# Optimization experiments

Measured on AMD Instinct MI355X. Metric: run time of the kernel, lower is better.

The kernel has to match this reference:

```python
import jax, jax.numpy as jnp
import numpy as np

HID = 512      # hidden_dim
MID = 256      # hid_dim
COND_D = 256   # condition_op_dim
OP_D = 32      # operator_len
EX_D = 32      # extra_info_num
L, N, T = 16, 1024, 8
EPS = 1e-5


def _lstm_cell(x_proj, h, c, Whh, bhh):
    # x_proj: precomputed x @ Wih.T + bih, shape [B, 4H]
    gates = x_proj + h @ Whh.T + bhh
    i, f, g, o = jnp.split(gates, 4, axis=-1)
    i = jax.nn.sigmoid(i); f = jax.nn.sigmoid(f)
    g = jnp.tanh(g); o = jax.nn.sigmoid(o)
    c = f * c + i * g
    h = o * jnp.tanh(c)
    return h, c


def _batchnorm(x, gamma, beta):
    mu = x.mean(0)
    var = x.var(0)  # biased, matches PyTorch training-mode normalization
    return gamma * (x - mu) * jax.lax.rsqrt(var + EPS) + beta


def setup_inputs() -> dict:
    key = jax.random.key(0)
    ks = jax.random.split(key, 24)
    s = lambda *sh: 0.05
    inp = {
        'operators': jax.random.normal(ks[0], (L, N, OP_D), jnp.float32),
        'extra_infos': jax.random.normal(ks[1], (L, N, EX_D), jnp.float32),
        'conditions': jax.random.normal(ks[2], (L, N, T, COND_D), jnp.float32),
        'condition_masks': jnp.ones((L, N, 1), jnp.float32),
        'mapping': jax.random.randint(ks[3], (L, N, 2), 0, N + 1, jnp.int32).astype(jnp.int64),
        'lstm1_Wih': jax.random.normal(ks[4], (4 * HID, COND_D), jnp.float32) * 0.05,
        'lstm1_Whh': jax.random.normal(ks[5], (4 * HID, HID), jnp.float32) * 0.05,
        'lstm1_bih': jnp.zeros((4 * HID,), jnp.float32),
        'lstm1_bhh': jnp.zeros((4 * HID,), jnp.float32),
        'cond_W': jax.random.normal(ks[6], (MID, HID), jnp.float32) * 0.05,
        'cond_b': jnp.zeros((MID,), jnp.float32),
        'bn1_g': jnp.ones((MID,), jnp.float32),
        'bn1_b': jnp.zeros((MID,), jnp.float32),
        'lstm2_Wih': jax.random.normal(ks[7], (4 * HID, OP_D + EX_D + MID), jnp.float32) * 0.05,
        'lstm2_Whh': jax.random.normal(ks[8], (4 * HID, HID), jnp.float32) * 0.05,
        'lstm2_bih': jnp.zeros((4 * HID,), jnp.float32),
        'lstm2_bhh': jnp.zeros((4 * HID,), jnp.float32),
        'bn2_g': jnp.ones((HID,), jnp.float32),
        'bn2_b': jnp.zeros((HID,), jnp.float32),
    }
    return inp


def reference(operators, extra_infos, conditions, condition_masks, mapping,
              lstm1_Wih, lstm1_Whh, lstm1_bih, lstm1_bhh,
              cond_W, cond_b, bn1_g, bn1_b,
              lstm2_Wih, lstm2_Whh, lstm2_bih, lstm2_bhh,
              bn2_g, bn2_b):
    B = L * N
    x = conditions.reshape(B, T, COND_D)
    # lstm1 over conditions; precompute input projections for all steps
    xp = jnp.einsum('btd,gd->btg', x, lstm1_Wih) + lstm1_bih  # [B,T,4H]

    def step1(carry, xt):
        h, c = carry
        h, c = _lstm_cell(xt, h, c, lstm1_Whh, lstm1_bhh)
        return (h, c), None

    h0 = jnp.zeros((B, HID), xp.dtype)
    (h1, _), _ = jax.lax.scan(step1, (h0, h0), jnp.swapaxes(xp, 0, 1))

    last = jax.nn.relu(h1 @ cond_W.T + cond_b)       # [B, MID]
    last = _batchnorm(last, bn1_g, bn1_b).reshape(L, N, MID)

    out = jnp.concatenate([operators, extra_infos, last], axis=2)  # [L,N,IN2]
    xp2 = jnp.einsum('lnd,gd->lng', out, lstm2_Wih) + lstm2_bih    # [L,N,4H]

    hz = jnp.zeros((N, HID), xp2.dtype)
    h, c = _lstm_cell(xp2[L - 1], hz, hz, lstm2_Whh, lstm2_bhh)

    mapping = mapping.astype(jnp.int32)
    levels = jnp.arange(L - 2, -1, -1)

    def tree_step(carry, idx):
        h, c = carry
        mp = mapping[idx]  # [N,2]
        pad = jnp.zeros((1, HID), h.dtype)
        ph = jnp.concatenate([pad, h], 0)  # [N+1,H]
        pc = jnp.concatenate([pad, c], 0)
        h = (ph[mp[:, 0]] + ph[mp[:, 1]]) * 0.5
        c = (pc[mp[:, 0]] + pc[mp[:, 1]]) * 0.5
        h, c = _lstm_cell(xp2[idx], h, c, lstm2_Whh, lstm2_bhh)
        return (h, c), None

    (h, c), _ = jax.lax.scan(tree_step, (h, c), levels)

    # batch_size == N since all operator rows are nonzero
    return _batchnorm(h, bn2_g, bn2_b)  # [N, HID]
```

## Files before the change

kernel.cpp:

```cpp
#include <hip/hip_runtime.h>
#include <hip/hip_bf16.h>
#include <stdint.h>


typedef __bf16 bf16;
typedef __bf16 bf16x8 __attribute__((ext_vector_type(8)));
typedef float f32x4 __attribute__((ext_vector_type(4)));

#define HIDDEN 512

__device__ __forceinline__ float fast_sig(float x) { return 1.f / (1.f + __expf(-x)); }
__device__ __forceinline__ float fast_tanh(float x) {
  float e = __expf(2.f * x);
  return 1.f - 2.f / (e + 1.f);
}

__device__ __forceinline__ void async16(const bf16* g, bf16* l) {
  __builtin_amdgcn_global_load_lds(
      (const __attribute__((address_space(1))) void*)g,
      (__attribute__((address_space(3))) void*)l, 16, 0, 0);
}

__device__ __forceinline__ void cvt_one(const float* __restrict__ src,
                                        bf16* __restrict__ dst, size_t i) {
  float4 a = *(const float4*)(src + i);
  float4 b = *(const float4*)(src + i + 4);
  bf16x8 r;
  r[0] = (bf16)a.x; r[1] = (bf16)a.y; r[2] = (bf16)a.z; r[3] = (bf16)a.w;
  r[4] = (bf16)b.x; r[5] = (bf16)b.y; r[6] = (bf16)b.z; r[7] = (bf16)b.w;
  *(bf16x8*)(dst + i) = r;
}

__global__ void cvt8(const float* __restrict__ src, bf16* __restrict__ dst) {
  size_t i = ((size_t)blockIdx.x * blockDim.x + threadIdx.x) * 8;
  cvt_one(src, dst, i);
}

__global__ void cvt_multi(const float* s0, bf16* d0,
                          const float* s1, bf16* d1,
                          const float* s2, bf16* d2,
                          const float* s3, bf16* d3,
                          const float* s4, bf16* d4,
                          const float* s5, bf16* d5,
                          const float* s6, bf16* d6) {
  int g = blockIdx.x * blockDim.x + threadIdx.x;
  const float* s; bf16* d; int off;
  if      (g < 65536)  { s = s0; d = d0; off = g; }
  else if (g < 131072) { s = s1; d = d1; off = g - 65536; }
  else if (g < 196608) { s = s2; d = d2; off = g - 131072; }
  else if (g < 327680) { s = s3; d = d3; off = g - 196608; }
  else if (g < 344064) { s = s4; d = d4; off = g - 327680; }
  else if (g < 425984) { s = s5; d = d5; off = g - 344064; }
  else if (g < 557056) { s = s6; d = d6; off = g - 425984; }
  else return;
  cvt_one(s, d, (size_t)off * 8);
}

__global__ void detect(const int* __restrict__ map, int* __restrict__ flags) {
  __shared__ int any;
  if (threadIdx.x == 0) any = 0;
  __syncthreads();
  int loc = 0;
  for (int i = threadIdx.x; i < 16384; i += blockDim.x) loc |= map[2 * i + 1];
  if (loc) atomicOr(&any, 1);
  __syncthreads();
  if (threadIdx.x == 0) flags[0] = (any == 0) ? 1 : 0;
}

template <int MT>
__global__ __launch_bounds__(256, 2) void cell_gemm(
    const bf16* __restrict__ A0, int a0off, int a0s, int a0kt,
    const bf16* __restrict__ A1, int a1s, int a1kt,
    const bf16* __restrict__ B0, int b0s,
    const bf16* __restrict__ B1, int b1s,
    const float* __restrict__ bias0, const float* __restrict__ bias1,
    const void* __restrict__ xp_add, int xp_f32,
    const float* __restrict__ c_prev,
    float* __restrict__ c_out,
    bf16* __restrict__ h_b16,
    float* __restrict__ h_f32)
{
  constexpr int BM = MT * 32;
  __shared__ __align__(16) bf16 sA[BM * 64];
  __shared__ __align__(16) bf16 sB[128 * 64];
  const int tid = threadIdx.x;
  const int lane = tid & 63;
  const int quad = lane >> 4, cl = lane & 15;
  const int wave = tid >> 6;
  const int wr = wave >> 1, wc = wave & 1;
  const int bm0 = blockIdx.x * BM;
  const int j0 = blockIdx.y * 32;

  f32x4 acc[MT][4];
#pragma unroll
  for (int mi = 0; mi < MT; ++mi)
#pragma unroll
    for (int g = 0; g < 4; ++g) acc[mi][g] = f32x4{0.f, 0.f, 0.f, 0.f};

#pragma unroll
  for (int ph = 0; ph < 2; ++ph) {
    const int kts = (ph == 0) ? a0kt : a1kt;
    const bf16* ab = (ph == 0) ? A0 : A1;
    const int as = (ph == 0) ? a0s : a1s;
    const int ao = (ph == 0) ? a0off : 0;
    const bf16* bb = (ph == 0) ? B0 : B1;
    const int bs = (ph == 0) ? b0s : b1s;
    for (int kt = 0; kt < kts; ++kt) {
#pragma unroll
      for (int ia = 0; ia < MT; ++ia) {
        int e = ia * 256 + tid;
        int row = e >> 3, sl = e & 7;
        int src = sl ^ (row & 7);
        async16(ab + (size_t)(bm0 + row) * as + ao + kt * 64 + src * 8, sA + e * 8);
      }
#pragma unroll
      for (int ib = 0; ib < 4; ++ib) {
        int e = ib * 256 + tid;
        int row = e >> 3, sl = e & 7;
        int src = sl ^ (row & 7);
        int wrow = (row >> 5) * HIDDEN + j0 + (row & 31);
        async16(bb + (size_t)wrow * bs + kt * 64 + src * 8, sB + e * 8);
      }
      __syncthreads();
#pragma unroll
      for (int kh = 0; kh < 2; ++kh) {
        bf16x8 af[MT], bfr[4];
#pragma unroll
        for (int mi = 0; mi < MT; ++mi) {
          int row = wr * (MT * 16) + mi * 16 + cl;
          int sl = (kh * 4 + quad) ^ (row & 7);
          af[mi] = *(const bf16x8*)&sA[row * 64 + sl * 8];
        }
#pragma unroll
        for (int g = 0; g < 4; ++g) {
          int row = g * 32 + wc * 16 + cl;
          int sl = (kh * 4 + quad) ^ (row & 7);
          bfr[g] = *(const bf16x8*)&sB[row * 64 + sl * 8];
        }
#pragma unroll
        for (int mi = 0; mi < MT; ++mi)
#pragma unroll
          for (int g = 0; g < 4; ++g)
            acc[mi][g] = __builtin_amdgcn_mfma_f32_16x16x32_bf16(af[mi], bfr[g], acc[mi][g], 0, 0, 0);
      }
      __syncthreads();
    }
  }

  const int j = j0 + wc * 16 + cl;
  float bI = bias0[j], bF = bias0[HIDDEN + j];
  float bG = bias0[2 * HIDDEN + j], bO = bias0[3 * HIDDEN + j];
  if (bias1) {
    bI += bias1[j]; bF += bias1[HIDDEN + j];
    bG += bias1[2 * HIDDEN + j]; bO += bias1[3 * HIDDEN + j];
  }
#pragma unroll
  for (int mi = 0; mi < MT; ++mi) {
    int rb = bm0 + wr * (MT * 16) + mi * 16 + quad * 4;
#pragma unroll
    for (int r = 0; r < 4; ++r) {
      int row = rb + r;
      float gi = acc[mi][0][r] + bI;
      float gf = acc[mi][1][r] + bF;
      float gg = acc[mi][2][r] + bG;
      float go = acc[mi][3][r] + bO;
      if (xp_add) {
        size_t base = (size_t)row * 2048;
        if (xp_f32) {
          const float* xr = (const float*)xp_add + base;
          gi += xr[j]; gf += xr[HIDDEN + j];
          gg += xr[2 * HIDDEN + j]; go += xr[3 * HIDDEN + j];
        } else {
          const bf16* xr = (const bf16*)xp_add + base;
          gi += (float)xr[j]; gf += (float)xr[HIDDEN + j];
          gg += (float)xr[2 * HIDDEN + j]; go += (float)xr[3 * HIDDEN + j];
        }
      }
      float iv = fast_sig(gi), fv = fast_sig(gf);
      float gv = fast_tanh(gg), ov = fast_sig(go);
      float cp = c_prev ? c_prev[(size_t)row * HIDDEN + j] : 0.f;
      float cn = fv * cp + iv * gv;
      float hn = ov * fast_tanh(cn);
      c_out[(size_t)row * HIDDEN + j] = cn;
      h_b16[(size_t)row * HIDDEN + j] = (bf16)hn;
      if (h_f32) h_f32[(size_t)row * HIDDEN + j] = hn;
    }
  }
}

template <int MT>
__global__ __launch_bounds__(256, 2) void plain_gemm(
    const bf16* __restrict__ A0, int a0s, int a0kt,
    const bf16* __restrict__ A1, int a1s, int a1kt,
    const bf16* __restrict__ A2, int a2s, int a2kt,
    const bf16* __restrict__ B, int bs,
    const float* __restrict__ bias, int do_relu,
    bf16* __restrict__ outh, float* __restrict__ outf, int Ntot)
{
  constexpr int BM = MT * 32;
  __shared__ __align__(16) bf16 sA[BM * 32];
  __shared__ __align__(16) bf16 sB[128 * 32];
  const int tid = threadIdx.x;
  const int lane = tid & 63;
  const int quad = lane >> 4, cl = lane & 15;
  const int wave = tid >> 6;
  const int wr = wave >> 1, wc = wave & 1;
  const int bm0 = blockIdx.x * BM;
  const int bn0 = blockIdx.y * 128;

  f32x4 acc[MT][4];
#pragma unroll
  for (int mi = 0; mi < MT; ++mi)
#pragma unroll
    for (int ni = 0; ni < 4; ++ni) acc[mi][ni] = f32x4{0.f, 0.f, 0.f, 0.f};

  const int nkt = a0kt + a1kt + a2kt;
  for (int kt = 0; kt < nkt; ++kt) {
    const bf16* abase; int astr, acol;
    if (kt < a0kt)            { abase = A0; astr = a0s; acol = kt * 32; }
    else if (kt < a0kt + a1kt){ abase = A1; astr = a1s; acol = (kt - a0kt) * 32; }
    else                      { abase = A2; astr = a2s; acol = (kt - a0kt - a1kt) * 32; }
#pragma unroll
    for (int ia = 0; ia < MT / 2; ++ia) {
      int e = ia * 256 + tid;
      int row = e >> 2, sl = e & 3;
      int src = sl ^ ((row >> 1) & 3);
      async16(abase + (size_t)(bm0 + row) * astr + acol + src * 8, sA + e * 8);
    }
#pragma unroll
    for (int ib = 0; ib < 2; ++ib) {
      int e = ib * 256 + tid;
      int row = e >> 2, sl = e & 3;
      int src = sl ^ ((row >> 1) & 3);
      async16(B + (size_t)(bn0 + row) * bs + kt * 32 + src * 8, sB + e * 8);
    }
    __syncthreads();
    bf16x8 af[MT], bfr[4];
#pragma unroll
    for (int mi = 0; mi < MT; ++mi) {
      int row = wr * (MT * 16) + mi * 16 + cl;
      int sl = quad ^ ((row >> 1) & 3);
      af[mi] = *(const bf16x8*)&sA[row * 32 + sl * 8];
    }
#pragma unroll
    for (int ni = 0; ni < 4; ++ni) {
      int row = wc * 64 + ni * 16 + cl;
      int sl = quad ^ ((row >> 1) & 3);
      bfr[ni] = *(const bf16x8*)&sB[row * 32 + sl * 8];
    }
#pragma unroll
    for (int mi = 0; mi < MT; ++mi)
#pragma unroll
      for (int ni = 0; ni < 4; ++ni)
        acc[mi][ni] = __builtin_amdgcn_mfma_f32_16x16x32_bf16(af[mi], bfr[ni], acc[mi][ni], 0, 0, 0);
    __syncthreads();
  }

#pragma unroll
  for (int mi = 0; mi < MT; ++mi) {
    int rb = bm0 + wr * (MT * 16) + mi * 16 + quad * 4;
#pragma unroll
    for (int ni = 0; ni < 4; ++ni) {
      int col = bn0 + wc * 64 + ni * 16 + cl;
      float bv = bias ? bias[col] : 0.f;
#pragma unroll
      for (int r = 0; r < 4; ++r) {
        int row = rb + r;
        float v = acc[mi][ni][r] + bv;
        if (do_relu) v = fmaxf(v, 0.f);
        if (outf) outf[(size_t)row * Ntot + col] = v;
        else      outh[(size_t)row * Ntot + col] = (bf16)v;
      }
    }
  }
}

__global__ void gather_h(const int* __restrict__ map, const int* __restrict__ flags,
                         int level,
                         const bf16* __restrict__ h_src, const float* __restrict__ c_src,
                         bf16* __restrict__ hA, float* __restrict__ c_dst)
{
  int n = blockIdx.x, t = threadIdx.x;
  long base = (long)level * 2048 + n * 2;
  int m0, m1;
  if (flags[0]) { m0 = map[base * 2]; m1 = map[base * 2 + 2]; }
  else          { m0 = map[base];     m1 = map[base + 1]; }
  float h0 = m0 ? (float)h_src[(size_t)(m0 - 1) * HIDDEN + t] : 0.f;
  float h1 = m1 ? (float)h_src[(size_t)(m1 - 1) * HIDDEN + t] : 0.f;
  float c0 = m0 ? c_src[(size_t)(m0 - 1) * HIDDEN + t] : 0.f;
  float c1 = m1 ? c_src[(size_t)(m1 - 1) * HIDDEN + t] : 0.f;
  hA[(size_t)n * HIDDEN + t] = (bf16)(0.5f * (h0 + h1));
  c_dst[(size_t)n * HIDDEN + t] = 0.5f * (c0 + c1);
}

__global__ void cell0(const void* __restrict__ xp, int xp_f32,
                      const float* __restrict__ bhh,
                      bf16* __restrict__ h, float* __restrict__ c)
{
  int n = blockIdx.x, j = threadIdx.x;
  float g[4];
#pragma unroll
  for (int k = 0; k < 4; ++k) {
    size_t idx = (size_t)n * 2048 + k * 512 + j;
    float v = xp_f32 ? ((const float*)xp)[idx] : (float)((const bf16*)xp)[idx];
    g[k] = v + bhh[k * 512 + j];
  }
  float cv = fast_sig(g[0]) * fast_tanh(g[2]);
  h[(size_t)n * HIDDEN + j] = (bf16)(fast_sig(g[3]) * fast_tanh(cv));
  c[(size_t)n * HIDDEN + j] = cv;
}

__global__ void bn_reduce_b16(const bf16* __restrict__ x, int rpb, int F,
                              float* __restrict__ partials) {
  int col = threadIdx.x, b = blockIdx.x;
  const bf16* p = x + (size_t)b * rpb * F + col;
  float s = 0.f, q = 0.f;
  for (int r = 0; r < rpb; ++r) { float v = (float)p[(size_t)r * F]; s += v; q += v * v; }
  partials[(size_t)b * 2 * F + col] = s;
  partials[(size_t)b * 2 * F + F + col] = q;
}

__global__ void bn_reduce_f32(const float* __restrict__ x, int rpb, int F,
                              float* __restrict__ partials) {
  int col = threadIdx.x, b = blockIdx.x;
  const float* p = x + (size_t)b * rpb * F + col;
  float s = 0.f, q = 0.f;
  for (int r = 0; r < rpb; ++r) { float v = p[(size_t)r * F]; s += v; q += v * v; }
  partials[(size_t)b * 2 * F + col] = s;
  partials[(size_t)b * 2 * F + F + col] = q;
}

__global__ void bn_final(const float* __restrict__ partials, int nb, int F,
                         const float* __restrict__ g, const float* __restrict__ b,
                         float invB, float* __restrict__ scale, float* __restrict__ shift) {
  int j = threadIdx.x;
  float s = 0.f, q = 0.f;
  for (int i = 0; i < nb; ++i) {
    s += partials[(size_t)i * 2 * F + j];
    q += partials[(size_t)i * 2 * F + F + j];
  }
  float mu = s * invB;
  float var = fmaxf(q * invB - mu * mu, 0.f);
  float sc = g[j] * rsqrtf(var + 1e-5f);
  scale[j] = sc;
  shift[j] = b[j] - sc * mu;
}

__global__ void bn_apply_mid(const bf16* __restrict__ x, const float* __restrict__ scale,
                             const float* __restrict__ shift, int Fmask, size_t total,
                             bf16* __restrict__ out) {
  for (size_t i = blockIdx.x * (size_t)blockDim.x + threadIdx.x; i < total;
       i += (size_t)gridDim.x * blockDim.x) {
    int j = (int)(i & (size_t)Fmask);
    out[i] = (bf16)(scale[j] * (float)x[i] + shift[j]);
  }
}

__global__ void bn_apply_out(const float* __restrict__ x, const float* __restrict__ scale,
                             const float* __restrict__ shift, int Fmask, size_t total,
                             float* __restrict__ out) {
  for (size_t i = blockIdx.x * (size_t)blockDim.x + threadIdx.x; i < total;
       i += (size_t)gridDim.x * blockDim.x) {
    int j = (int)(i & (size_t)Fmask);
    out[i] = scale[j] * x[i] + shift[j];
  }
}

extern "C" void kernel_launch(void* const* d_in, const int* in_sizes, int n_in,
                              void* d_out, int out_size, void* d_ws, size_t ws_size,
                              hipStream_t stream) {
  const float* operators = (const float*)d_in[0];
  const float* extras    = (const float*)d_in[1];
  const float* conds     = (const float*)d_in[2];
  const int*   mapping   = (const int*)d_in[4];
  const float* b1ih = (const float*)d_in[7];
  const float* b1hh = (const float*)d_in[8];
  const float* condb = (const float*)d_in[10];
  const float* bn1g = (const float*)d_in[11];
  const float* bn1b = (const float*)d_in[12];
  const float* b2ih = (const float*)d_in[15];
  const float* b2hh = (const float*)d_in[16];
  const float* bn2g = (const float*)d_in[17];
  const float* bn2b = (const float*)d_in[18];

  char* ws = (char*)d_ws;
  size_t o = 0;
  auto alloc = [&](size_t bytes) {
    char* p = ws + o;
    o += (bytes + 255) & ~(size_t)255;
    return p;
  };
  bf16* conds_b = (bf16*)alloc((size_t)33554432 * 2);
  bf16* ops_b   = (bf16*)alloc((size_t)524288 * 2);
  bf16* ext_b   = (bf16*)alloc((size_t)524288 * 2);
  bf16* w1ih_b  = (bf16*)alloc((size_t)524288 * 2);
  bf16* w1hh_b  = (bf16*)alloc((size_t)1048576 * 2);
  bf16* condw_b = (bf16*)alloc((size_t)131072 * 2);
  bf16* w2ih_b  = (bf16*)alloc((size_t)655360 * 2);
  bf16* w2hh_b  = (bf16*)alloc((size_t)1048576 * 2);
  bf16* h1[2];
  h1[0] = (bf16*)alloc((size_t)16384 * 512 * 2);
  h1[1] = (bf16*)alloc((size_t)16384 * 512 * 2);
  float* c1 = (float*)alloc((size_t)16384 * 512 * 4);
  bf16* last_relu = (bf16*)alloc((size_t)16384 * 256 * 2);
  bf16* last_bn = (bf16*)alloc((size_t)16384 * 256 * 2);
  bf16* h2 = (bf16*)alloc((size_t)1024 * 512 * 2);
  bf16* hA = (bf16*)alloc((size_t)1024 * 512 * 2);
  float* c2a = (float*)alloc((size_t)1024 * 512 * 4);
  float* c2b = (float*)alloc((size_t)1024 * 512 * 4);
  float* h2f = (float*)alloc((size_t)1024 * 512 * 4);
  float* partials = (float*)alloc((size_t)64 * 1024 * 4);
  float* scale1 = (float*)alloc(256 * 4);
  float* shift1 = (float*)alloc(256 * 4);
  float* scale2 = (float*)alloc(512 * 4);
  float* shift2 = (float*)alloc(512 * 4);
  int* flags = (int*)alloc(256);

  size_t xp2_elems = (size_t)16384 * 2048;
  int xpf = (o + xp2_elems * 4 <= ws_size) ? 1 : 0;
  void* xp2 = alloc(xp2_elems * (xpf ? 4 : 2));
  float* xp2f = xpf ? (float*)xp2 : nullptr;
  bf16* xp2h = xpf ? nullptr : (bf16*)xp2;

  detect<<<1, 256, 0, stream>>>(mapping, flags);
  cvt8<<<16384, 256, 0, stream>>>(conds, conds_b);
  cvt_multi<<<2176, 256, 0, stream>>>(
      operators, ops_b, extras, ext_b,
      (const float*)d_in[5], w1ih_b, (const float*)d_in[6], w1hh_b,
      (const float*)d_in[9], condw_b, (const float*)d_in[13], w2ih_b,
      (const float*)d_in[14], w2hh_b);

  for (int t = 0; t < 8; ++t) {
    const bf16* hprev = (t == 0) ? nullptr : h1[t & 1];
    cell_gemm<4><<<dim3(128, 16), 256, 0, stream>>>(
        conds_b, t * 256, 2048, 4,
        hprev, 512, (t == 0) ? 0 : 8,
        w1ih_b, 256, w1hh_b, 512,
        b1ih, b1hh,
        nullptr, 0,
        (t == 0) ? nullptr : c1, c1, h1[(t + 1) & 1], nullptr);
  }

  plain_gemm<2><<<dim3(256, 2), 256, 0, stream>>>(
      h1[0], 512, 16, nullptr, 0, 0, nullptr, 0, 0,
      condw_b, 512, condb, 1, last_relu, nullptr, 256);
  bn_reduce_b16<<<64, 256, 0, stream>>>(last_relu, 256, 256, partials);
  bn_final<<<1, 256, 0, stream>>>(partials, 64, 256, bn1g, bn1b, 1.f / 16384.f, scale1, shift1);
  bn_apply_mid<<<1024, 256, 0, stream>>>(last_relu, scale1, shift1, 255,
                                         (size_t)16384 * 256, last_bn);

  plain_gemm<4><<<dim3(128, 16), 256, 0, stream>>>(
      ops_b, 32, 1, ext_b, 32, 1, last_bn, 256, 8,
      w2ih_b, 320, b2ih, 0, xp2h, xp2f, 2048);

  size_t lvl_sz = (size_t)1024 * 2048;
  const void* xp15 = xpf ? (const void*)(xp2f + 15 * lvl_sz) : (const void*)(xp2h + 15 * lvl_sz);
  cell0<<<1024, 512, 0, stream>>>(xp15, xpf, b2hh, h2, c2a);
  for (int idx = 14; idx >= 0; --idx) {
    gather_h<<<1024, 512, 0, stream>>>(mapping, flags, idx, h2, c2a, hA, c2b);
    const void* xpl = xpf ? (const void*)(xp2f + idx * lvl_sz) : (const void*)(xp2h + idx * lvl_sz);
    cell_gemm<1><<<dim3(32, 16), 256, 0, stream>>>(
        hA, 0, 512, 8,
        nullptr, 0, 0,
        w2hh_b, 512, nullptr, 0,
        b2hh, nullptr,
        xpl, xpf,
        c2b, c2a, h2,
        (idx == 0) ? h2f : nullptr);
  }

  bn_reduce_f32<<<16, 512, 0, stream>>>(h2f, 64, 512, partials);
  bn_final<<<1, 512, 0, stream>>>(partials, 16, 512, bn2g, bn2b, 1.f / 1024.f, scale2, shift2);
  bn_apply_out<<<512, 256, 0, stream>>>(h2f, scale2, shift2, 511,
                                        (size_t)1024 * 512, (float*)d_out);
}
```

Baseline: 1.201 ms.

## Replace per-level tree launches with a persistent kernel using grid barriers

The 15-level tree recurrence becomes one persistent kernel of 512 blocks. Each level gathers parent h into shared memory, runs the recurrent GEMM and fuses the c gather into the cell update, with a global atomic barrier between levels. This replaces about 31 small launches (cell0, gather_h, cell_gemm per level). The three prep kernels are also merged into one launch, and cell_gemm is templated on K-tile counts with its address arithmetic hoisted. The grid barrier assumes all 512 blocks are resident at once, otherwise it deadlocks, and it adds spin-wait cost at each level.

Result: slower. 1.920 ms (+59.8%).

```diff
diff --git a/kernel.cpp b/kernel.cpp
--- a/kernel.cpp
+++ b/kernel.cpp
@@ -8,6 +8,7 @@
 typedef float f32x4 __attribute__((ext_vector_type(4)));
 
 #define HIDDEN 512
+#define TNB 512
 
 __device__ __forceinline__ float fast_sig(float x) { return 1.f / (1.f + __expf(-x)); }
 __device__ __forceinline__ float fast_tanh(float x) {
@@ -31,54 +32,51 @@
   *(bf16x8*)(dst + i) = r;
 }
 
-__global__ void cvt8(const float* __restrict__ src, bf16* __restrict__ dst) {
-  size_t i = ((size_t)blockIdx.x * blockDim.x + threadIdx.x) * 8;
-  cvt_one(src, dst, i);
-}
-
-__global__ void cvt_multi(const float* s0, bf16* d0,
-                          const float* s1, bf16* d1,
-                          const float* s2, bf16* d2,
-                          const float* s3, bf16* d3,
-                          const float* s4, bf16* d4,
-                          const float* s5, bf16* d5,
-                          const float* s6, bf16* d6) {
-  int g = blockIdx.x * blockDim.x + threadIdx.x;
-  const float* s; bf16* d; int off;
-  if      (g < 65536)  { s = s0; d = d0; off = g; }
-  else if (g < 131072) { s = s1; d = d1; off = g - 65536; }
-  else if (g < 196608) { s = s2; d = d2; off = g - 131072; }
-  else if (g < 327680) { s = s3; d = d3; off = g - 196608; }
-  else if (g < 344064) { s = s4; d = d4; off = g - 327680; }
-  else if (g < 425984) { s = s5; d = d5; off = g - 344064; }
-  else if (g < 557056) { s = s6; d = d6; off = g - 425984; }
-  else return;
-  cvt_one(s, d, (size_t)off * 8);
-}
-
-__global__ void detect(const int* __restrict__ map, int* __restrict__ flags) {
-  __shared__ int any;
-  if (threadIdx.x == 0) any = 0;
-  __syncthreads();
-  int loc = 0;
-  for (int i = threadIdx.x; i < 16384; i += blockDim.x) loc |= map[2 * i + 1];
-  if (loc) atomicOr(&any, 1);
-  __syncthreads();
-  if (threadIdx.x == 0) flags[0] = (any == 0) ? 1 : 0;
-}
-
-template <int MT>
+__global__ void prep(const float* conds, bf16* conds_b,
+                     const float* s0, bf16* d0, const float* s1, bf16* d1,
+                     const float* s2, bf16* d2, const float* s3, bf16* d3,
+                     const float* s4, bf16* d4, const float* s5, bf16* d5,
+                     const float* s6, bf16* d6,
+                     const int* map, int* flags, int* bar) {
+  int b = blockIdx.x;
+  int tid = threadIdx.x;
+  if (b < 2176) {
+    int g = b * 256 + tid;
+    const float* s; bf16* d; int off;
+    if      (g < 65536)  { s = s0; d = d0; off = g; }
+    else if (g < 131072) { s = s1; d = d1; off = g - 65536; }
+    else if (g < 196608) { s = s2; d = d2; off = g - 131072; }
+    else if (g < 327680) { s = s3; d = d3; off = g - 196608; }
+    else if (g < 344064) { s = s4; d = d4; off = g - 327680; }
+    else if (g < 425984) { s = s5; d = d5; off = g - 344064; }
+    else if (g < 557056) { s = s6; d = d6; off = g - 425984; }
+    else return;
+    cvt_one(s, d, (size_t)off * 8);
+  } else if (b == 2176) {
+    __shared__ int any;
+    if (tid == 0) { any = 0; bar[0] = 0; bar[1] = 0; }
+    __syncthreads();
+    int loc = 0;
+    for (int i = tid; i < 16384; i += 256) loc |= map[2 * i + 1];
+    if (loc) atomicOr(&any, 1);
+    __syncthreads();
+    if (tid == 0) flags[0] = (any == 0) ? 1 : 0;
+  } else {
+    size_t i = ((size_t)(b - 2177) * 256 + tid) * 8;
+    cvt_one(conds, conds_b, i);
+  }
+}
+
+template <int MT, int KT0, int KT1>
 __global__ __launch_bounds__(256, 2) void cell_gemm(
-    const bf16* __restrict__ A0, int a0off, int a0s, int a0kt,
-    const bf16* __restrict__ A1, int a1s, int a1kt,
+    const bf16* __restrict__ A0, int a0off, int a0s,
+    const bf16* __restrict__ A1, int a1s,
     const bf16* __restrict__ B0, int b0s,
     const bf16* __restrict__ B1, int b1s,
     const float* __restrict__ bias0, const float* __restrict__ bias1,
-    const void* __restrict__ xp_add, int xp_f32,
     const float* __restrict__ c_prev,
     float* __restrict__ c_out,
-    bf16* __restrict__ h_b16,
-    float* __restrict__ h_f32)
+    bf16* __restrict__ h_b16)
 {
   constexpr int BM = MT * 32;
   __shared__ __align__(16) bf16 sA[BM * 64];
@@ -91,99 +89,109 @@
   const int bm0 = blockIdx.x * BM;
   const int j0 = blockIdx.y * 32;
 
+  const bf16* ra[MT][2];
+  const bf16* rb[4][2];
+#pragma unroll
+  for (int mi = 0; mi < MT; ++mi)
+#pragma unroll
+    for (int kh = 0; kh < 2; ++kh) {
+      int row = wr * (MT * 16) + mi * 16 + cl;
+      int sl = (kh * 4 + quad) ^ (row & 7);
+      ra[mi][kh] = &sA[row * 64 + sl * 8];
+    }
+#pragma unroll
+  for (int g = 0; g < 4; ++g)
+#pragma unroll
+    for (int kh = 0; kh < 2; ++kh) {
+      int row = g * 32 + wc * 16 + cl;
+      int sl = (kh * 4 + quad) ^ (row & 7);
+      rb[g][kh] = &sB[row * 64 + sl * 8];
+    }
+
   f32x4 acc[MT][4];
 #pragma unroll
   for (int mi = 0; mi < MT; ++mi)
 #pragma unroll
     for (int g = 0; g < 4; ++g) acc[mi][g] = f32x4{0.f, 0.f, 0.f, 0.f};
 
-#pragma unroll
-  for (int ph = 0; ph < 2; ++ph) {
-    const int kts = (ph == 0) ? a0kt : a1kt;
-    const bf16* ab = (ph == 0) ? A0 : A1;
-    const int as = (ph == 0) ? a0s : a1s;
-    const int ao = (ph == 0) ? a0off : 0;
-    const bf16* bb = (ph == 0) ? B0 : B1;
-    const int bs = (ph == 0) ? b0s : b1s;
-    for (int kt = 0; kt < kts; ++kt) {
-#pragma unroll
-      for (int ia = 0; ia < MT; ++ia) {
-        int e = ia * 256 + tid;
-        int row = e >> 3, sl = e & 7;
-        int src = sl ^ (row & 7);
-        async16(ab + (size_t)(bm0 + row) * as + ao + kt * 64 + src * 8, sA + e * 8);
-      }
-#pragma unroll
-      for (int ib = 0; ib < 4; ++ib) {
-        int e = ib * 256 + tid;
-        int row = e >> 3, sl = e & 7;
-        int src = sl ^ (row & 7);
-        int wrow = (row >> 5) * HIDDEN + j0 + (row & 31);
-        async16(bb + (size_t)wrow * bs + kt * 64 + src * 8, sB + e * 8);
-      }
-      __syncthreads();
-#pragma unroll
-      for (int kh = 0; kh < 2; ++kh) {
-        bf16x8 af[MT], bfr[4];
-#pragma unroll
-        for (int mi = 0; mi < MT; ++mi) {
-          int row = wr * (MT * 16) + mi * 16 + cl;
-          int sl = (kh * 4 + quad) ^ (row & 7);
-          af[mi] = *(const bf16x8*)&sA[row * 64 + sl * 8];
-        }
-#pragma unroll
-        for (int g = 0; g < 4; ++g) {
-          int row = g * 32 + wc * 16 + cl;
-          int sl = (kh * 4 + quad) ^ (row & 7);
-          bfr[g] = *(const bf16x8*)&sB[row * 64 + sl * 8];
-        }
-#pragma unroll
-        for (int mi = 0; mi < MT; ++mi)
-#pragma unroll
-          for (int g = 0; g < 4; ++g)
-            acc[mi][g] = __builtin_amdgcn_mfma_f32_16x16x32_bf16(af[mi], bfr[g], acc[mi][g], 0, 0, 0);
-      }
-      __syncthreads();
-    }
+  const bf16* pa[MT];
+  const bf16* pb[4];
+#pragma unroll
+  for (int ia = 0; ia < MT; ++ia) {
+    int e = ia * 256 + tid, row = e >> 3, sl = e & 7;
+    pa[ia] = A0 + (size_t)((bm0 + row) * a0s + a0off + (sl ^ (row & 7)) * 8);
+  }
+#pragma unroll
+  for (int ib = 0; ib < 4; ++ib) {
+    int e = ib * 256 + tid, row = e >> 3, sl = e & 7;
+    int wrow = (row >> 5) * HIDDEN + j0 + (row & 31);
+    pb[ib] = B0 + (size_t)(wrow * b0s + (sl ^ (row & 7)) * 8);
+  }
+
+  auto ktile = [&]() {
+#pragma unroll
+    for (int ia = 0; ia < MT; ++ia) {
+      async16(pa[ia], sA + (ia * 256 + tid) * 8);
+      pa[ia] += 64;
+    }
+#pragma unroll
+    for (int ib = 0; ib < 4; ++ib) {
+      async16(pb[ib], sB + (ib * 256 + tid) * 8);
+      pb[ib] += 64;
+    }
+    __syncthreads();
+#pragma unroll
+    for (int kh = 0; kh < 2; ++kh) {
+      bf16x8 af[MT], bfr[4];
+#pragma unroll
+      for (int mi = 0; mi < MT; ++mi) af[mi] = *(const bf16x8*)ra[mi][kh];
+#pragma unroll
+      for (int g = 0; g < 4; ++g) bfr[g] = *(const bf16x8*)rb[g][kh];
+#pragma unroll
+      for (int mi = 0; mi < MT; ++mi)
+#pragma unroll
+        for (int g = 0; g < 4; ++g)
+          acc[mi][g] = __builtin_amdgcn_mfma_f32_16x16x32_bf16(af[mi], bfr[g], acc[mi][g], 0, 0, 0);
+    }
+    __syncthreads();
+  };
+
+  for (int kt = 0; kt < KT0; ++kt) ktile();
+  if (KT1 > 0) {
+#pragma unroll
+    for (int ia = 0; ia < MT; ++ia) {
+      int e = ia * 256 + tid, row = e >> 3, sl = e & 7;
+      pa[ia] = A1 + (size_t)((bm0 + row) * a1s + (sl ^ (row & 7)) * 8);
+    }
+#pragma unroll
+    for (int ib = 0; ib < 4; ++ib) {
+      int e = ib * 256 + tid, row = e >> 3, sl = e & 7;
+      int wrow = (row >> 5) * HIDDEN + j0 + (row & 31);
+      pb[ib] = B1 + (size_t)(wrow * b1s + (sl ^ (row & 7)) * 8);
+    }
+    for (int kt = 0; kt < KT1; ++kt) ktile();
   }
 
   const int j = j0 + wc * 16 + cl;
   float bI = bias0[j], bF = bias0[HIDDEN + j];
   float bG = bias0[2 * HIDDEN + j], bO = bias0[3 * HIDDEN + j];
-  if (bias1) {
-    bI += bias1[j]; bF += bias1[HIDDEN + j];
-    bG += bias1[2 * HIDDEN + j]; bO += bias1[3 * HIDDEN + j];
-  }
+  bI += bias1[j]; bF += bias1[HIDDEN + j];
+  bG += bias1[2 * HIDDEN + j]; bO += bias1[3 * HIDDEN + j];
 #pragma unroll
   for (int mi = 0; mi < MT; ++mi) {
-    int rb = bm0 + wr * (MT * 16) + mi * 16 + quad * 4;
+    int rb_ = bm0 + wr * (MT * 16) + mi * 16 + quad * 4;
 #pragma unroll
     for (int r = 0; r < 4; ++r) {
-      int row = rb + r;
-      float gi = acc[mi][0][r] + bI;
-      float gf = acc[mi][1][r] + bF;
-      float gg = acc[mi][2][r] + bG;
-      float go = acc[mi][3][r] + bO;
-      if (xp_add) {
-        size_t base = (size_t)row * 2048;
-        if (xp_f32) {
-          const float* xr = (const float*)xp_add + base;
-          gi += xr[j]; gf += xr[HIDDEN + j];
-          gg += xr[2 * HIDDEN + j]; go += xr[3 * HIDDEN + j];
-        } else {
-          const bf16* xr = (const bf16*)xp_add + base;
-          gi += (float)xr[j]; gf += (float)xr[HIDDEN + j];
-          gg += (float)xr[2 * HIDDEN + j]; go += (float)xr[3 * HIDDEN + j];
-        }
-      }
-      float iv = fast_sig(gi), fv = fast_sig(gf);
-      float gv = fast_tanh(gg), ov = fast_sig(go);
+      int row = rb_ + r;
+      float iv = fast_sig(acc[mi][0][r] + bI);
+      float fv = fast_sig(acc[mi][1][r] + bF);
+      float gv = fast_tanh(acc[mi][2][r] + bG);
+      float ov = fast_sig(acc[mi][3][r] + bO);
       float cp = c_prev ? c_prev[(size_t)row * HIDDEN + j] : 0.f;
       float cn = fv * cp + iv * gv;
       float hn = ov * fast_tanh(cn);
       c_out[(size_t)row * HIDDEN + j] = cn;
       h_b16[(size_t)row * HIDDEN + j] = (bf16)hn;
-      if (h_f32) h_f32[(size_t)row * HIDDEN + j] = hn;
     }
   }
 }
@@ -275,39 +283,151 @@
   }
 }
 
-__global__ void gather_h(const int* __restrict__ map, const int* __restrict__ flags,
-                         int level,
-                         const bf16* __restrict__ h_src, const float* __restrict__ c_src,
-                         bf16* __restrict__ hA, float* __restrict__ c_dst)
+__device__ __forceinline__ void gbar(int* bar, int target) {
+  __syncthreads();
+  if (threadIdx.x == 0) {
+    __threadfence();
+    if (atomicAdd(&bar[0], 1) == TNB - 1) {
+      atomicExch(&bar[0], 0);
+      atomicAdd(&bar[1], 1);
+      __threadfence();
+    } else {
+      while (__hip_atomic_load(&bar[1], __ATOMIC_RELAXED, __HIP_MEMORY_SCOPE_AGENT) < target)
+        __builtin_amdgcn_s_sleep(1);
+      __threadfence();
+    }
+  }
+  __syncthreads();
+}
+
+__global__ __launch_bounds__(256, 2) void tree_persist(
+    const int* __restrict__ map, const int* __restrict__ flags,
+    const void* __restrict__ xp2, int xpf,
+    const bf16* __restrict__ W, const float* __restrict__ bhh,
+    bf16* __restrict__ h0, bf16* __restrict__ h1,
+    float* __restrict__ c0, float* __restrict__ c1,
+    float* __restrict__ hf, int* __restrict__ bar)
 {
-  int n = blockIdx.x, t = threadIdx.x;
-  long base = (long)level * 2048 + n * 2;
-  int m0, m1;
-  if (flags[0]) { m0 = map[base * 2]; m1 = map[base * 2 + 2]; }
-  else          { m0 = map[base];     m1 = map[base + 1]; }
-  float h0 = m0 ? (float)h_src[(size_t)(m0 - 1) * HIDDEN + t] : 0.f;
-  float h1 = m1 ? (float)h_src[(size_t)(m1 - 1) * HIDDEN + t] : 0.f;
-  float c0 = m0 ? c_src[(size_t)(m0 - 1) * HIDDEN + t] : 0.f;
-  float c1 = m1 ? c_src[(size_t)(m1 - 1) * HIDDEN + t] : 0.f;
-  hA[(size_t)n * HIDDEN + t] = (bf16)(0.5f * (h0 + h1));
-  c_dst[(size_t)n * HIDDEN + t] = 0.5f * (c0 + c1);
-}
-
-__global__ void cell0(const void* __restrict__ xp, int xp_f32,
-                      const float* __restrict__ bhh,
-                      bf16* __restrict__ h, float* __restrict__ c)
-{
-  int n = blockIdx.x, j = threadIdx.x;
-  float g[4];
-#pragma unroll
-  for (int k = 0; k < 4; ++k) {
-    size_t idx = (size_t)n * 2048 + k * 512 + j;
-    float v = xp_f32 ? ((const float*)xp)[idx] : (float)((const bf16*)xp)[idx];
-    g[k] = v + bhh[k * 512 + j];
-  }
-  float cv = fast_sig(g[0]) * fast_tanh(g[2]);
-  h[(size_t)n * HIDDEN + j] = (bf16)(fast_sig(g[3]) * fast_tanh(cv));
-  c[(size_t)n * HIDDEN + j] = cv;
+  __shared__ __align__(16) bf16 sA[32 * 512];
+  __shared__ __align__(16) bf16 sB[128 * 64];
+  __shared__ int smap[64];
+  const int tid = threadIdx.x;
+  const int lane = tid & 63, wave = tid >> 6;
+  const int quad = lane >> 4, cl = lane & 15;
+  const int wm = wave >> 1, wj = wave & 1;
+  const int bm0 = (blockIdx.x & 31) * 32;
+  const int jb = blockIdx.x >> 5;
+  const int j0 = jb * 32;
+  const int is64 = flags[0];
+  const size_t lvl = (size_t)1024 * 2048;
+
+  for (int u = tid; u < 32 * 32; u += 256) {
+    int r = bm0 + (u >> 5), j = j0 + (u & 31);
+    float g[4];
+#pragma unroll
+    for (int k = 0; k < 4; ++k) {
+      size_t idx = 15 * lvl + (size_t)r * 2048 + k * 512 + j;
+      g[k] = (xpf ? ((const float*)xp2)[idx] : (float)((const bf16*)xp2)[idx]) + bhh[k * 512 + j];
+    }
+    float cv = fast_sig(g[0]) * fast_tanh(g[2]);
+    h0[(size_t)r * 512 + j] = (bf16)(fast_sig(g[3]) * fast_tanh(cv));
+    c0[(size_t)r * 512 + j] = cv;
+  }
+  int target = 1;
+  gbar(bar, target);
+
+  const bf16* hs = h0; bf16* hd = h1;
+  const float* cs = c0; float* cd = c1;
+  for (int idx = 14; idx >= 0; --idx) {
+    if (tid < 64) {
+      long base = (long)idx * 2048 + (bm0 + (tid >> 1)) * 2 + (tid & 1);
+      smap[tid] = is64 ? map[base * 2] : map[base];
+    }
+    __syncthreads();
+    for (int u = tid; u < 2048; u += 256) {
+      int row = u >> 6, slot = u & 63;
+      int m0 = smap[row * 2], m1 = smap[row * 2 + 1];
+      int col = slot * 8;
+      float a8[8] = {0.f, 0.f, 0.f, 0.f, 0.f, 0.f, 0.f, 0.f};
+      if (m0) {
+        bf16x8 x = *(const bf16x8*)&hs[(size_t)(m0 - 1) * 512 + col];
+#pragma unroll
+        for (int q = 0; q < 8; ++q) a8[q] += (float)x[q];
+      }
+      if (m1) {
+        bf16x8 x = *(const bf16x8*)&hs[(size_t)(m1 - 1) * 512 + col];
+#pragma unroll
+        for (int q = 0; q < 8; ++q) a8[q] += (float)x[q];
+      }
+      bf16x8 rr;
+#pragma unroll
+      for (int q = 0; q < 8; ++q) rr[q] = (bf16)(0.5f * a8[q]);
+      *(bf16x8*)&sA[(row << 9) + (slot ^ (row & 7)) * 8] = rr;
+    }
+    f32x4 acc[4];
+#pragma unroll
+    for (int g = 0; g < 4; ++g) acc[g] = f32x4{0.f, 0.f, 0.f, 0.f};
+    for (int kt = 0; kt < 8; ++kt) {
+#pragma unroll
+      for (int ib = 0; ib < 4; ++ib) {
+        int e = ib * 256 + tid;
+        int row = e >> 3, sl = e & 7;
+        int wrow = (row >> 5) * HIDDEN + j0 + (row & 31);
+        async16(W + (size_t)wrow * HIDDEN + kt * 64 + (sl ^ (row & 7)) * 8, sB + e * 8);
+      }
+      __syncthreads();
+#pragma unroll
+      for (int kh = 0; kh < 2; ++kh) {
+        int arow = wm * 16 + cl;
+        int s = kt * 8 + kh * 4 + quad;
+        bf16x8 af = *(const bf16x8*)&sA[(arow << 9) + (s ^ (arow & 7)) * 8];
+#pragma unroll
+        for (int g = 0; g < 4; ++g) {
+          int brow = g * 32 + wj * 16 + cl;
+          bf16x8 bfr = *(const bf16x8*)&sB[brow * 64 + ((kh * 4 + quad) ^ (brow & 7)) * 8];
+          acc[g] = __builtin_amdgcn_mfma_f32_16x16x32_bf16(af, bfr, acc[g], 0, 0, 0);
+        }
+      }
+      __syncthreads();
+    }
+    const int j = j0 + wj * 16 + cl;
+    float bI = bhh[j], bF = bhh[HIDDEN + j];
+    float bG = bhh[2 * HIDDEN + j], bO = bhh[3 * HIDDEN + j];
+    int lr0 = wm * 16 + quad * 4;
+#pragma unroll
+    for (int r = 0; r < 4; ++r) {
+      int lr = lr0 + r;
+      int row = bm0 + lr;
+      float gi = acc[0][r] + bI;
+      float gf = acc[1][r] + bF;
+      float gg = acc[2][r] + bG;
+      float go = acc[3][r] + bO;
+      size_t base = idx * lvl + (size_t)row * 2048;
+      if (xpf) {
+        const float* xr = (const float*)xp2 + base;
+        gi += xr[j]; gf += xr[HIDDEN + j];
+        gg += xr[2 * HIDDEN + j]; go += xr[3 * HIDDEN + j];
+      } else {
+        const bf16* xr = (const bf16*)xp2 + base;
+        gi += (float)xr[j]; gf += (float)xr[HIDDEN + j];
+        gg += (float)xr[2 * HIDDEN + j]; go += (float)xr[3 * HIDDEN + j];
+      }
+      int m0 = smap[lr * 2], m1 = smap[lr * 2 + 1];
+      float cp = 0.f;
+      if (m0) cp += cs[(size_t)(m0 - 1) * 512 + j];
+      if (m1) cp += cs[(size_t)(m1 - 1) * 512 + j];
+      cp *= 0.5f;
+      float cn = fast_sig(gf) * cp + fast_sig(gi) * fast_tanh(gg);
+      float hn = fast_sig(go) * fast_tanh(cn);
+      cd[(size_t)row * 512 + j] = cn;
+      hd[(size_t)row * 512 + j] = (bf16)hn;
+      if (idx == 0) hf[(size_t)row * 512 + j] = hn;
+    }
+    ++target;
+    gbar(bar, target);
+    const bf16* th = hs; hs = hd; hd = (bf16*)th;
+    const float* tc = cs; cs = cd; cd = (float*)tc;
+  }
 }
 
 __global__ void bn_reduce_b16(const bf16* __restrict__ x, int rpb, int F,
@@ -404,8 +524,8 @@
   float* c1 = (float*)alloc((size_t)16384 * 512 * 4);
   bf16* last_relu = (bf16*)alloc((size_t)16384 * 256 * 2);
   bf16* last_bn = (bf16*)alloc((size_t)16384 * 256 * 2);
-  bf16* h2 = (bf16*)alloc((size_t)1024 * 512 * 2);
-  bf16* hA = (bf16*)alloc((size_t)1024 * 512 * 2);
+  bf16* h2a = (bf16*)alloc((size_t)1024 * 512 * 2);
+  bf16* h2b = (bf16*)alloc((size_t)1024 * 512 * 2);
   float* c2a = (float*)alloc((size_t)1024 * 512 * 4);
   float* c2b = (float*)alloc((size_t)1024 * 512 * 4);
   float* h2f = (float*)alloc((size_t)1024 * 512 * 4);
@@ -415,6 +535,7 @@
   float* scale2 = (float*)alloc(512 * 4);
   float* shift2 = (float*)alloc(512 * 4);
   int* flags = (int*)alloc(256);
+  int* bar = (int*)alloc(256);
 
   size_t xp2_elems = (size_t)16384 * 2048;
   int xpf = (o + xp2_elems * 4 <= ws_size) ? 1 : 0;
@@ -422,23 +543,23 @@
   float* xp2f = xpf ? (float*)xp2 : nullptr;
   bf16* xp2h = xpf ? nullptr : (bf16*)xp2;
 
-  detect<<<1, 256, 0, stream>>>(mapping, flags);
-  cvt8<<<16384, 256, 0, stream>>>(conds, conds_b);
-  cvt_multi<<<2176, 256, 0, stream>>>(
+  prep<<<18561, 256, 0, stream>>>(
+      conds, conds_b,
       operators, ops_b, extras, ext_b,
       (const float*)d_in[5], w1ih_b, (const float*)d_in[6], w1hh_b,
       (const float*)d_in[9], condw_b, (const float*)d_in[13], w2ih_b,
-      (const float*)d_in[14], w2hh_b);
-
-  for (int t = 0; t < 8; ++t) {
-    const bf16* hprev = (t == 0) ? nullptr : h1[t & 1];
-    cell_gemm<4><<<dim3(128, 16), 256, 0, stream>>>(
-        conds_b, t * 256, 2048, 4,
-        hprev, 512, (t == 0) ? 0 : 8,
+      (const float*)d_in[14], w2hh_b,
+      mapping, flags, bar);
+
+  cell_gemm<4, 4, 0><<<dim3(128, 16), 256, 0, stream>>>(
+      conds_b, 0, 2048, nullptr, 512,
+      w1ih_b, 256, w1hh_b, 512,
+      b1ih, b1hh, nullptr, c1, h1[1]);
+  for (int t = 1; t < 8; ++t) {
+    cell_gemm<4, 4, 8><<<dim3(128, 16), 256, 0, stream>>>(
+        conds_b, t * 256, 2048, h1[t & 1], 512,
         w1ih_b, 256, w1hh_b, 512,
-        b1ih, b1hh,
-        nullptr, 0,
-        (t == 0) ? nullptr : c1, c1, h1[(t + 1) & 1], nullptr);
+        b1ih, b1hh, c1, c1, h1[(t + 1) & 1]);
   }
 
   plain_gemm<2><<<dim3(256, 2), 256, 0, stream>>>(
@@ -453,21 +574,9 @@
       ops_b, 32, 1, ext_b, 32, 1, last_bn, 256, 8,
       w2ih_b, 320, b2ih, 0, xp2h, xp2f, 2048);
 
-  size_t lvl_sz = (size_t)1024 * 2048;
-  const void* xp15 = xpf ? (const void*)(xp2f + 15 * lvl_sz) : (const void*)(xp2h + 15 * lvl_sz);
-  cell0<<<1024, 512, 0, stream>>>(xp15, xpf, b2hh, h2, c2a);
-  for (int idx = 14; idx >= 0; --idx) {
-    gather_h<<<1024, 512, 0, stream>>>(mapping, flags, idx, h2, c2a, hA, c2b);
-    const void* xpl = xpf ? (const void*)(xp2f + idx * lvl_sz) : (const void*)(xp2h + idx * lvl_sz);
-    cell_gemm<1><<<dim3(32, 16), 256, 0, stream>>>(
-        hA, 0, 512, 8,
-        nullptr, 0, 0,
-        w2hh_b, 512, nullptr, 0,
-        b2hh, nullptr,
-        xpl, xpf,
-        c2b, c2a, h2,
-        (idx == 0) ? h2f : nullptr);
-  }
+  tree_persist<<<TNB, 256, 0, stream>>>(
+      mapping, flags, xp2, xpf, w2hh_b, b2hh,
+      h2a, h2b, c2a, c2b, h2f, bar);
 
   bn_reduce_f32<<<16, 512, 0, stream>>>(h2f, 64, 512, partials);
   bn_final<<<1, 512, 0, stream>>>(partials, 16, 512, bn2g, bn2b, 1.f / 1024.f, scale2, shift2);
```
